# Kernel tuning notes

Measured on AMD Instinct MI355X. Metric: run time of the kernel, lower is better.

The kernel has to match this reference:

```python
import jax, jax.numpy as jnp
import numpy as np

N = 10000      # total nodes
E = 320000     # total edges (avg degree 32)
T = 8          # time steps
F = 32         # feature width (in = hidden = out)
L = 3          # len(hidden_sizes) + 1 layers
EPS = 1e-5     # BatchNorm eps


def setup_inputs() -> dict:
    key = jax.random.key(0)
    ks = jax.random.split(key, 6)
    node_features = jax.random.normal(ks[0], (N, F), dtype=jnp.float32)
    edges_weight = jax.random.uniform(ks[1], (T, E), dtype=jnp.float32)
    src = jax.random.randint(ks[2], (E,), 0, N, dtype=jnp.int32)
    dst = jax.random.randint(ks[3], (E,), 0, N, dtype=jnp.int32)
    Ws = jax.random.normal(ks[4], (L, F, F), dtype=jnp.float32) / np.float32(np.sqrt(F))
    bs = jnp.zeros((L, F), dtype=jnp.float32)
    gammas = jnp.ones((L, F), dtype=jnp.float32)
    betas = jnp.zeros((L, F), dtype=jnp.float32)
    return dict(node_features=node_features, edges_weight=edges_weight,
                src=src, dst=dst, Ws=Ws, bs=bs, gammas=gammas, betas=betas)


def reference(node_features, edges_weight, src, dst, Ws, bs, gammas, betas):
    w_et = edges_weight.T            # (E, T), matches edge_weights.t()
    n = node_features.shape[0]
    h = node_features                # (N, F) first layer, (N, T, F) after
    for l in range(L):
        hs = h[src]                  # gather source-node features
        if hs.ndim == 2:
            hs = hs[:, None, :]      # (E, 1, F) -> broadcast over T
        msg = hs * w_et[:, :, None]  # u_mul_e: (E, T, F)
        agg = jax.ops.segment_sum(msg, dst, num_segments=n)  # sum per dst: (N, T, F)
        out = jnp.einsum('ntf,of->nto', agg, Ws[l]) + bs[l]  # Linear
        # BatchNorm1d (training mode): stats over (N, T) per channel, biased var
        mean = out.mean(axis=(0, 1))
        var = out.var(axis=(0, 1))
        out = (out - mean) * jax.lax.rsqrt(var + EPS) * gammas[l] + betas[l]
        h = jax.nn.relu(out)
    return h                         # (N, T, F)
```

## Files before the change

### kernel.cpp

```cpp
#include <hip/hip_runtime.h>

#define TF 8
#define FD 32
#define EPSV 1e-5f

__device__ __forceinline__ void atomAddF(float* p, float v) {
#if defined(__HIP_PLATFORM_AMD__)
    unsafeAtomicAdd(p, v);
#else
    atomicAdd(p, v);
#endif
}

__global__ __launch_bounds__(256) void hist_kernel(
    const int* __restrict__ dst, int* __restrict__ counts, int E)
{
    int e = blockIdx.x * 256 + threadIdx.x;
    if (e < E) atomicAdd(&counts[dst[e]], 1);
}

__global__ __launch_bounds__(1024) void scan_kernel(
    const int* __restrict__ counts, int* __restrict__ rowptr,
    int* __restrict__ cursor, int Nn)
{
    __shared__ int totals[1024];
    int tid = threadIdx.x;
    int per = (Nn + 1023) >> 10;
    int start = tid * per;
    int end = min(start + per, Nn);
    if (end < start) end = start;
    int s = 0;
    for (int i = start; i < end; ++i) s += counts[i];
    totals[tid] = s;
    __syncthreads();
    for (int off = 1; off < 1024; off <<= 1) {
        int t2 = (tid >= off) ? totals[tid - off] : 0;
        __syncthreads();
        totals[tid] += t2;
        __syncthreads();
    }
    int running = totals[tid] - s;
    for (int i = start; i < end; ++i) {
        rowptr[i] = running;
        cursor[i] = running;
        running += counts[i];
    }
    if (tid == 1023) rowptr[Nn] = totals[1023];
}

__global__ __launch_bounds__(256) void fillA_kernel(
    const int* __restrict__ src, const int* __restrict__ dst,
    const float* __restrict__ w, int* __restrict__ cursor,
    int* __restrict__ ssrc, float* __restrict__ ws8, int E)
{
    int e = blockIdx.x * 256 + threadIdx.x;
    if (e >= E) return;
    int d = dst[e];
    int j = atomicAdd(&cursor[d], 1);
    ssrc[j] = src[e];
    #pragma unroll
    for (int t = 0; t < TF; ++t)
        ws8[(size_t)j * TF + t] = w[(size_t)t * E + e];
}

template <int MODE>
__global__ __launch_bounds__(256) void agg_gemm2_kernel(
    const float* __restrict__ h, const float* __restrict__ coefIn,
    const int* __restrict__ rowptr, const int* __restrict__ ssrc,
    const float* __restrict__ ws8,
    const float* __restrict__ W, const float* __restrict__ bias,
    float* __restrict__ out, float* __restrict__ stats)
{
    __shared__ float Wt[FD * FD];
    __shared__ float red[8 * TF * FD];
    int tid = threadIdx.x;
    int slot = tid >> 5, f = tid & 31;
    {
        int ff = tid & 31;
        Wt[ff * FD + (tid >> 5)] = W[tid];
        Wt[ff * FD + ((tid + 256) >> 5)] = W[tid + 256];
        Wt[ff * FD + ((tid + 512) >> 5)] = W[tid + 512];
        Wt[ff * FD + ((tid + 768) >> 5)] = W[tid + 768];
    }
    float cA = 0.f, cB = 0.f;
    if (MODE == 1) { cA = coefIn[f]; cB = coefIn[FD + f]; }

    int node = blockIdx.x;
    int rs = rowptr[node], re = rowptr[node + 1];

    float acc[TF];
    #pragma unroll
    for (int t = 0; t < TF; ++t) acc[t] = 0.f;

    int j = rs + slot;
    int s = (j < re) ? ssrc[j] : 0;
    for (; j < re; j += 8) {
        int jn = j + 8;
        int s_next = (jn < re) ? ssrc[jn] : 0;
        float4 wA = *(const float4*)(ws8 + (size_t)j * TF);
        float4 wB = *(const float4*)(ws8 + (size_t)j * TF + 4);
        if (MODE == 0) {
            float hv = h[(size_t)s * FD + f];
            acc[0] = fmaf(wA.x, hv, acc[0]);
            acc[1] = fmaf(wA.y, hv, acc[1]);
            acc[2] = fmaf(wA.z, hv, acc[2]);
            acc[3] = fmaf(wA.w, hv, acc[3]);
            acc[4] = fmaf(wB.x, hv, acc[4]);
            acc[5] = fmaf(wB.y, hv, acc[5]);
            acc[6] = fmaf(wB.z, hv, acc[6]);
            acc[7] = fmaf(wB.w, hv, acc[7]);
        } else {
            const float* hp = h + (size_t)s * (TF * FD) + f;
            float hv[TF];
            #pragma unroll
            for (int t = 0; t < TF; ++t) hv[t] = hp[t * FD];
            #pragma unroll
            for (int t = 0; t < TF; ++t) {
                float hn = fmaxf(0.f, fmaf(hv[t], cA, cB));
                float wv = (t == 0) ? wA.x : (t == 1) ? wA.y : (t == 2) ? wA.z :
                           (t == 3) ? wA.w : (t == 4) ? wB.x : (t == 5) ? wB.y :
                           (t == 6) ? wB.z : wB.w;
                acc[t] = fmaf(wv, hn, acc[t]);
            }
        }
        s = s_next;
    }
    #pragma unroll
    for (int t = 0; t < TF; ++t)
        red[slot * (TF * FD) + t * FD + f] = acc[t];
    __syncthreads();
    int t2 = tid >> 5;
    float asum = 0.f;
    #pragma unroll
    for (int sl = 0; sl < 8; ++sl)
        asum += red[sl * (TF * FD) + t2 * FD + f];
    __syncthreads();
    red[t2 * FD + f] = asum;
    __syncthreads();

    float oval = bias[f];
    #pragma unroll
    for (int k = 0; k < FD; ++k)
        oval = fmaf(red[t2 * FD + k], Wt[k * FD + f], oval);
    out[(size_t)node * (TF * FD) + tid] = oval;

    __syncthreads();
    red[tid] = oval;
    red[256 + tid] = oval * oval;
    __syncthreads();
    #pragma unroll
    for (int stride = 128; stride >= 32; stride >>= 1) {
        if (tid < stride) {
            red[tid] += red[tid + stride];
            red[256 + tid] += red[256 + tid + stride];
        }
        __syncthreads();
    }
    if (tid < 32) {
        int slot2 = blockIdx.x & 31;
        atomAddF(&stats[slot2 * 64 + tid], red[tid]);
        atomAddF(&stats[slot2 * 64 + 32 + tid], red[256 + tid]);
    }
}

__global__ void finalize_kernel(const float* __restrict__ stats,
                                const float* __restrict__ gamma,
                                const float* __restrict__ beta,
                                float* __restrict__ coef, float inv_count)
{
    int o = threadIdx.x;
    float s = 0.f, sq = 0.f;
    #pragma unroll
    for (int k = 0; k < 32; ++k) { s += stats[k * 64 + o]; sq += stats[k * 64 + 32 + o]; }
    float mean = s * inv_count;
    float var  = sq * inv_count - mean * mean;
    float sc   = gamma[o] * rsqrtf(var + EPSV);
    coef[o]      = sc;
    coef[FD + o] = beta[o] - mean * sc;
}

__global__ __launch_bounds__(256) void norm_relu_kernel(
    float* __restrict__ x, const float* __restrict__ coef, int n4)
{
    int gid = blockIdx.x * 256 + threadIdx.x;
    if (gid >= n4) return;
    float4 v = ((const float4*)x)[gid];
    int o = (gid * 4) & 31;
    float4 r;
    r.x = fmaxf(0.f, fmaf(v.x, coef[o],     coef[32 + o]));
    r.y = fmaxf(0.f, fmaf(v.y, coef[o + 1], coef[33 + o]));
    r.z = fmaxf(0.f, fmaf(v.z, coef[o + 2], coef[34 + o]));
    r.w = fmaxf(0.f, fmaf(v.w, coef[o + 3], coef[35 + o]));
    ((float4*)x)[gid] = r;
}

__global__ __launch_bounds__(256) void scatter0_kernel(
    const float* __restrict__ h, const float* __restrict__ w,
    const int* __restrict__ src, const int* __restrict__ dst,
    float* __restrict__ agg, int E)
{
    int gid = blockIdx.x * 256 + threadIdx.x;
    int e = gid >> 5;
    if (e >= E) return;
    int f = gid & 31;
    int s = src[e], d = dst[e];
    float hv = h[(size_t)s * FD + f];
    float* aggd = agg + (size_t)d * (TF * FD) + f;
    #pragma unroll
    for (int t = 0; t < TF; ++t)
        atomAddF(aggd + t * FD, w[(size_t)t * E + e] * hv);
}

__global__ __launch_bounds__(256) void scatterL_kernel(
    const float* __restrict__ h, const float* __restrict__ w,
    const int* __restrict__ src, const int* __restrict__ dst,
    float* __restrict__ agg, int E)
{
    int gid = blockIdx.x * 256 + threadIdx.x;
    int e = gid >> 5;
    if (e >= E) return;
    int f = gid & 31;
    int s = src[e], d = dst[e];
    const float* hs = h + (size_t)s * (TF * FD) + f;
    float* aggd = agg + (size_t)d * (TF * FD) + f;
    #pragma unroll
    for (int t = 0; t < TF; ++t)
        atomAddF(aggd + t * FD, w[(size_t)t * E + e] * hs[t * FD]);
}

__global__ __launch_bounds__(256) void gemm_stats_kernel(
    const float* __restrict__ agg, const float* __restrict__ W,
    const float* __restrict__ bias, float* __restrict__ out,
    float* __restrict__ stats, int nrows)
{
    __shared__ float Wt[FD * FD];
    __shared__ float rows[8 * FD];
    int tid = threadIdx.x;
    for (int i = tid; i < FD * FD; i += 256) {
        int o = i >> 5, f = i & 31;
        Wt[f * FD + o] = W[i];
    }
    int o = tid & 31;
    int r = tid >> 5;
    float b = bias[o];
    float sum = 0.f, sumsq = 0.f;
    int ngroups = (nrows + 7) >> 3;
    for (int g = blockIdx.x; g < ngroups; g += gridDim.x) {
        int row0 = g * 8;
        __syncthreads();
        int idx = row0 * FD + tid;
        rows[tid] = (idx < nrows * FD) ? agg[idx] : 0.f;
        __syncthreads();
        int row = row0 + r;
        if (row < nrows) {
            float acc = b;
            #pragma unroll
            for (int f2 = 0; f2 < FD; ++f2)
                acc = fmaf(rows[r * FD + f2], Wt[f2 * FD + o], acc);
            out[(size_t)row * FD + o] = acc;
            sum += acc;
            sumsq += acc * acc;
        }
    }
    __syncthreads();
    rows[tid] = sum;
    Wt[tid] = sumsq;
    __syncthreads();
    for (int stride = 128; stride >= 32; stride >>= 1) {
        if (tid < stride) { rows[tid] += rows[tid + stride]; Wt[tid] += Wt[tid + stride]; }
        __syncthreads();
    }
    if (tid < 32) {
        int slot = blockIdx.x & 31;
        atomAddF(&stats[slot * 64 + tid], rows[tid]);
        atomAddF(&stats[slot * 64 + 32 + tid], Wt[tid]);
    }
}

extern "C" void kernel_launch(void* const* d_in, const int* in_sizes, int n_in,
                              void* d_out, int out_size, void* d_ws, size_t ws_size,
                              hipStream_t stream)
{
    const float* nf  = (const float*)d_in[0];
    const float* wgt = (const float*)d_in[1];
    const int*   src = (const int*)d_in[2];
    const int*   dst = (const int*)d_in[3];
    const float* Ws  = (const float*)d_in[4];
    const float* bs  = (const float*)d_in[5];
    const float* gam = (const float*)d_in[6];
    const float* bet = (const float*)d_in[7];

    int E  = in_sizes[2];
    int Nn = in_sizes[0] / FD;
    int nrows = Nn * TF;
    int n4 = nrows * FD / 4;
    float inv_count = 1.0f / (float)nrows;
    float* out = (float*)d_out;

    size_t idxInts = (size_t)(3 * Nn + 4);
    size_t hbufF   = (size_t)nrows * FD;
    size_t needA = (idxInts + (size_t)E + (size_t)E * TF + hbufF + 3 * 2048 + 3 * 64) * 4;

    int eb = (E + 255) / 256;

    if (ws_size >= needA) {
        int*   counts = (int*)d_ws;
        int*   cursor = counts + Nn;
        int*   rowptr = cursor + Nn;
        int*   ssrc   = counts + idxInts;
        float* ws8    = (float*)(ssrc + E);
        float* hbuf   = ws8 + (size_t)E * TF;
        float* stats  = hbuf + hbufF;
        float* coef   = stats + 3 * 2048;

        hipMemsetAsync(counts, 0, (size_t)Nn * sizeof(int), stream);
        hipMemsetAsync(stats, 0, 3 * 2048 * sizeof(float), stream);
        hist_kernel<<<eb, 256, 0, stream>>>(dst, counts, E);
        scan_kernel<<<1, 1024, 0, stream>>>(counts, rowptr, cursor, Nn);
        fillA_kernel<<<eb, 256, 0, stream>>>(src, dst, wgt, cursor, ssrc, ws8, E);

        agg_gemm2_kernel<0><<<Nn, 256, 0, stream>>>(
            nf, nullptr, rowptr, ssrc, ws8, Ws, bs, out, stats);
        finalize_kernel<<<1, 32, 0, stream>>>(
            stats, gam, bet, coef, inv_count);
        agg_gemm2_kernel<1><<<Nn, 256, 0, stream>>>(
            out, coef, rowptr, ssrc, ws8, Ws + FD * FD, bs + FD,
            hbuf, stats + 2048);
        finalize_kernel<<<1, 32, 0, stream>>>(
            stats + 2048, gam + FD, bet + FD, coef + 64, inv_count);
        agg_gemm2_kernel<1><<<Nn, 256, 0, stream>>>(
            hbuf, coef + 64, rowptr, ssrc, ws8, Ws + 2 * FD * FD, bs + 2 * FD,
            out, stats + 2 * 2048);
        finalize_kernel<<<1, 32, 0, stream>>>(
            stats + 2 * 2048, gam + 2 * FD, bet + 2 * FD, coef + 2 * 64, inv_count);
        norm_relu_kernel<<<(n4 + 255) / 256, 256, 0, stream>>>(out, coef + 2 * 64, n4);
    } else {
        float* agg   = (float*)d_ws;
        float* stats = agg + (size_t)nrows * FD;
        float* coef  = stats + 2048;
        int scatterBlocks = (E * 32 + 255) / 256;
        for (int l = 0; l < 3; ++l) {
            hipMemsetAsync(agg, 0, (size_t)nrows * FD * sizeof(float), stream);
            hipMemsetAsync(stats, 0, 2048 * sizeof(float), stream);
            if (l == 0)
                scatter0_kernel<<<scatterBlocks, 256, 0, stream>>>(nf, wgt, src, dst, agg, E);
            else
                scatterL_kernel<<<scatterBlocks, 256, 0, stream>>>(out, wgt, src, dst, agg, E);
            gemm_stats_kernel<<<2048, 256, 0, stream>>>(
                agg, Ws + l * FD * FD, bs + l * FD, out, stats, nrows);
            finalize_kernel<<<1, 32, 0, stream>>>(
                stats, gam + l * FD, bet + l * FD, coef, inv_count);
            norm_relu_kernel<<<(n4 + 255) / 256, 256, 0, stream>>>(out, coef, n4);
        }
    }
}
```

Measured before the change: 261.7 us.

## Store edge weights and intermediate activations as packed bf16 with feature-major layout

Edge weights are packed to bf16 (8 time steps in one uint4 per edge) during the CSR fill. Intermediate hidden activations between layers are also stored as bf16, in a layout where each (node, feature) pair holds all 8 time steps in one 16-byte word. Gathers then need one vector load instead of eight strided scalar loads. This cuts memory traffic in the gather-bound aggregation kernels, at the cost of bf16 rounding error in the weights and hidden states, which may exceed the tolerance.

New measurement: 251.2 us. 1.04x faster.

```diff
diff --git a/kernel.cpp b/kernel.cpp
--- a/kernel.cpp
+++ b/kernel.cpp
@@ -10,6 +10,14 @@
 #else
     atomicAdd(p, v);
 #endif
+}
+
+__device__ __forceinline__ unsigned int f2bfu(float x) {
+    unsigned int u = __float_as_uint(x);
+    return (u + 0x7FFFu + ((u >> 16) & 1u)) >> 16;
+}
+__device__ __forceinline__ float bfx(unsigned int w, int hi) {
+    return __uint_as_float(hi ? (w & 0xFFFF0000u) : (w << 16));
 }
 
 __global__ __launch_bounds__(256) void hist_kernel(
@@ -51,28 +59,34 @@
 __global__ __launch_bounds__(256) void fillA_kernel(
     const int* __restrict__ src, const int* __restrict__ dst,
     const float* __restrict__ w, int* __restrict__ cursor,
-    int* __restrict__ ssrc, float* __restrict__ ws8, int E)
+    int* __restrict__ ssrc, uint4* __restrict__ wsb, int E)
 {
     int e = blockIdx.x * 256 + threadIdx.x;
     if (e >= E) return;
     int d = dst[e];
     int j = atomicAdd(&cursor[d], 1);
     ssrc[j] = src[e];
-    #pragma unroll
-    for (int t = 0; t < TF; ++t)
-        ws8[(size_t)j * TF + t] = w[(size_t)t * E + e];
-}
-
-template <int MODE>
-__global__ __launch_bounds__(256) void agg_gemm2_kernel(
-    const float* __restrict__ h, const float* __restrict__ coefIn,
+    uint4 p;
+    p.x = f2bfu(w[(size_t)0 * E + e]) | (f2bfu(w[(size_t)1 * E + e]) << 16);
+    p.y = f2bfu(w[(size_t)2 * E + e]) | (f2bfu(w[(size_t)3 * E + e]) << 16);
+    p.z = f2bfu(w[(size_t)4 * E + e]) | (f2bfu(w[(size_t)5 * E + e]) << 16);
+    p.w = f2bfu(w[(size_t)6 * E + e]) | (f2bfu(w[(size_t)7 * E + e]) << 16);
+    wsb[j] = p;
+}
+
+template <int MODE, int OUTB>
+__global__ __launch_bounds__(256) void agg_gemm3_kernel(
+    const float* __restrict__ hf, const uint4* __restrict__ hb,
+    const float* __restrict__ coefIn,
     const int* __restrict__ rowptr, const int* __restrict__ ssrc,
-    const float* __restrict__ ws8,
+    const uint4* __restrict__ wsb,
     const float* __restrict__ W, const float* __restrict__ bias,
-    float* __restrict__ out, float* __restrict__ stats)
+    unsigned int* __restrict__ outU, float* __restrict__ outF,
+    float* __restrict__ stats)
 {
     __shared__ float Wt[FD * FD];
-    __shared__ float red[8 * TF * FD];
+    __shared__ float red[512];
+    __shared__ float pacc[8 * TF * FD];
     int tid = threadIdx.x;
     int slot = tid >> 5, f = tid & 31;
     {
@@ -97,57 +111,57 @@
     for (; j < re; j += 8) {
         int jn = j + 8;
         int s_next = (jn < re) ? ssrc[jn] : 0;
-        float4 wA = *(const float4*)(ws8 + (size_t)j * TF);
-        float4 wB = *(const float4*)(ws8 + (size_t)j * TF + 4);
+        uint4 wp = wsb[j];
+        unsigned int ww[4] = { wp.x, wp.y, wp.z, wp.w };
         if (MODE == 0) {
-            float hv = h[(size_t)s * FD + f];
-            acc[0] = fmaf(wA.x, hv, acc[0]);
-            acc[1] = fmaf(wA.y, hv, acc[1]);
-            acc[2] = fmaf(wA.z, hv, acc[2]);
-            acc[3] = fmaf(wA.w, hv, acc[3]);
-            acc[4] = fmaf(wB.x, hv, acc[4]);
-            acc[5] = fmaf(wB.y, hv, acc[5]);
-            acc[6] = fmaf(wB.z, hv, acc[6]);
-            acc[7] = fmaf(wB.w, hv, acc[7]);
+            float hv = hf[(size_t)s * FD + f];
+            #pragma unroll
+            for (int t = 0; t < TF; ++t)
+                acc[t] = fmaf(bfx(ww[t >> 1], t & 1), hv, acc[t]);
         } else {
-            const float* hp = h + (size_t)s * (TF * FD) + f;
-            float hv[TF];
-            #pragma unroll
-            for (int t = 0; t < TF; ++t) hv[t] = hp[t * FD];
+            uint4 hp = hb[(size_t)s * FD + f];
+            unsigned int hw[4] = { hp.x, hp.y, hp.z, hp.w };
             #pragma unroll
             for (int t = 0; t < TF; ++t) {
-                float hn = fmaxf(0.f, fmaf(hv[t], cA, cB));
-                float wv = (t == 0) ? wA.x : (t == 1) ? wA.y : (t == 2) ? wA.z :
-                           (t == 3) ? wA.w : (t == 4) ? wB.x : (t == 5) ? wB.y :
-                           (t == 6) ? wB.z : wB.w;
-                acc[t] = fmaf(wv, hn, acc[t]);
+                float hr = bfx(hw[t >> 1], t & 1);
+                float hn = fmaxf(0.f, fmaf(hr, cA, cB));
+                acc[t] = fmaf(bfx(ww[t >> 1], t & 1), hn, acc[t]);
             }
         }
         s = s_next;
     }
     #pragma unroll
     for (int t = 0; t < TF; ++t)
-        red[slot * (TF * FD) + t * FD + f] = acc[t];
+        pacc[slot * (TF * FD) + t * FD + f] = acc[t];
     __syncthreads();
     int t2 = tid >> 5;
     float asum = 0.f;
     #pragma unroll
     for (int sl = 0; sl < 8; ++sl)
-        asum += red[sl * (TF * FD) + t2 * FD + f];
-    __syncthreads();
-    red[t2 * FD + f] = asum;
+        asum += pacc[sl * (TF * FD) + t2 * FD + f];
+    red[tid] = asum;
     __syncthreads();
 
     float oval = bias[f];
     #pragma unroll
     for (int k = 0; k < FD; ++k)
         oval = fmaf(red[t2 * FD + k], Wt[k * FD + f], oval);
-    out[(size_t)node * (TF * FD) + tid] = oval;
+    if (!OUTB)
+        outF[(size_t)node * (TF * FD) + tid] = oval;
 
     __syncthreads();
     red[tid] = oval;
     red[256 + tid] = oval * oval;
     __syncthreads();
+    if (OUTB) {
+        if (tid < 128) {
+            int ff = tid >> 2, q = tid & 3;
+            unsigned int lo = f2bfu(red[(q * 2) * FD + ff]);
+            unsigned int hi = f2bfu(red[(q * 2 + 1) * FD + ff]);
+            outU[(size_t)node * 128 + ff * 4 + q] = lo | (hi << 16);
+        }
+        __syncthreads();
+    }
     #pragma unroll
     for (int stride = 128; stride >= 32; stride >>= 1) {
         if (tid < stride) {
@@ -298,39 +312,40 @@
     float* out = (float*)d_out;
 
     size_t idxInts = (size_t)(3 * Nn + 4);
-    size_t hbufF   = (size_t)nrows * FD;
-    size_t needA = (idxInts + (size_t)E + (size_t)E * TF + hbufF + 3 * 2048 + 3 * 64) * 4;
+    size_t needW = (idxInts + (size_t)E + 4 * (size_t)E + 128 * (size_t)Nn * 2
+                    + 3 * 2048 + 3 * 64) * 4;
 
     int eb = (E + 255) / 256;
 
-    if (ws_size >= needA) {
-        int*   counts = (int*)d_ws;
-        int*   cursor = counts + Nn;
-        int*   rowptr = cursor + Nn;
-        int*   ssrc   = counts + idxInts;
-        float* ws8    = (float*)(ssrc + E);
-        float* hbuf   = ws8 + (size_t)E * TF;
-        float* stats  = hbuf + hbufF;
-        float* coef   = stats + 3 * 2048;
+    if (ws_size >= needW) {
+        int*          counts = (int*)d_ws;
+        int*          cursor = counts + Nn;
+        int*          rowptr = cursor + Nn;
+        int*          ssrc   = counts + idxInts;
+        uint4*        wsb    = (uint4*)(ssrc + E);
+        unsigned int* hb0    = (unsigned int*)(wsb + E);
+        unsigned int* hb1    = hb0 + (size_t)Nn * 128;
+        float*        stats  = (float*)(hb1 + (size_t)Nn * 128);
+        float*        coef   = stats + 3 * 2048;
 
         hipMemsetAsync(counts, 0, (size_t)Nn * sizeof(int), stream);
         hipMemsetAsync(stats, 0, 3 * 2048 * sizeof(float), stream);
         hist_kernel<<<eb, 256, 0, stream>>>(dst, counts, E);
         scan_kernel<<<1, 1024, 0, stream>>>(counts, rowptr, cursor, Nn);
-        fillA_kernel<<<eb, 256, 0, stream>>>(src, dst, wgt, cursor, ssrc, ws8, E);
-
-        agg_gemm2_kernel<0><<<Nn, 256, 0, stream>>>(
-            nf, nullptr, rowptr, ssrc, ws8, Ws, bs, out, stats);
-        finalize_kernel<<<1, 32, 0, stream>>>(
-            stats, gam, bet, coef, inv_count);
-        agg_gemm2_kernel<1><<<Nn, 256, 0, stream>>>(
-            out, coef, rowptr, ssrc, ws8, Ws + FD * FD, bs + FD,
-            hbuf, stats + 2048);
+        fillA_kernel<<<eb, 256, 0, stream>>>(src, dst, wgt, cursor, ssrc, wsb, E);
+
+        agg_gemm3_kernel<0, 1><<<Nn, 256, 0, stream>>>(
+            nf, nullptr, nullptr, rowptr, ssrc, wsb, Ws, bs,
+            hb0, nullptr, stats);
+        finalize_kernel<<<1, 32, 0, stream>>>(stats, gam, bet, coef, inv_count);
+        agg_gemm3_kernel<1, 1><<<Nn, 256, 0, stream>>>(
+            nullptr, (const uint4*)hb0, coef, rowptr, ssrc, wsb,
+            Ws + FD * FD, bs + FD, hb1, nullptr, stats + 2048);
         finalize_kernel<<<1, 32, 0, stream>>>(
             stats + 2048, gam + FD, bet + FD, coef + 64, inv_count);
-        agg_gemm2_kernel<1><<<Nn, 256, 0, stream>>>(
-            hbuf, coef + 64, rowptr, ssrc, ws8, Ws + 2 * FD * FD, bs + 2 * FD,
-            out, stats + 2 * 2048);
+        agg_gemm3_kernel<1, 0><<<Nn, 256, 0, stream>>>(
+            nullptr, (const uint4*)hb1, coef + 64, rowptr, ssrc, wsb,
+            Ws + 2 * FD * FD, bs + 2 * FD, nullptr, out, stats + 2 * 2048);
         finalize_kernel<<<1, 32, 0, stream>>>(
             stats + 2 * 2048, gam + 2 * FD, bet + 2 * FD, coef + 2 * 64, inv_count);
         norm_relu_kernel<<<(n4 + 255) / 256, 256, 0, stream>>>(out, coef + 2 * 64, n4);
```
